# Kernel tuning notes

Measured on AMD Instinct MI355X. Metric: run time of the kernel, lower is better.

Reference implementation:

```python
import jax, jax.numpy as jnp
import numpy as np

B, S, E, H, M, Q = 2, 2048, 768, 12, 768, 4
D = E // H  # head_dim = 64
EPS = 1e-5


def _layernorm(x, g, b):
    m = jnp.mean(x, axis=-1, keepdims=True)
    v = jnp.mean((x - m) ** 2, axis=-1, keepdims=True)
    return (x - m) / jnp.sqrt(v + EPS) * g + b


def setup_inputs() -> dict:
    key = jax.random.key(0)
    ks = jax.random.split(key, 12)
    w = lambda k, shape, s=0.02: (jax.random.normal(k, shape) * s).astype(jnp.float32)
    return {
        "x": jax.random.normal(ks[0], (B, S, E), dtype=jnp.float32),
        "ln1_g": jnp.ones((E,), jnp.float32), "ln1_b": jnp.zeros((E,), jnp.float32),
        "wq": w(ks[1], (E, E)), "bq": jnp.zeros((E,), jnp.float32),
        "wk": w(ks[2], (E, E)), "bk": jnp.zeros((E,), jnp.float32),
        "wv": w(ks[3], (E, E)), "bv": jnp.zeros((E,), jnp.float32),
        "wo": w(ks[4], (E, E)), "bo": jnp.zeros((E,), jnp.float32),
        "ln2_g": jnp.ones((E,), jnp.float32), "ln2_b": jnp.zeros((E,), jnp.float32),
        "w1": w(ks[5], (E, Q * M)), "b1": jnp.zeros((Q * M,), jnp.float32),
        "wvqc": w(ks[6], (M, M)), "bvqc": jnp.zeros((M,), jnp.float32),
        "w2": w(ks[7], (Q * M, E)), "b2": jnp.zeros((E,), jnp.float32),
    }


def reference(x, ln1_g, ln1_b, wq, bq, wk, bk, wv, bv, wo, bo,
              ln2_g, ln2_b, w1, b1, wvqc, bvqc, w2, b2):
    b, s, e = x.shape
    h, d = H, e // H

    # --- attention branch (pre-norm, per-query-L2-normalized logits) ---
    xn = _layernorm(x, ln1_g, ln1_b)
    q = (xn @ wq + bq).reshape(b, s, h, d).transpose(0, 2, 1, 3)  # bhsd
    k = (xn @ wk + bk).reshape(b, s, h, d).transpose(0, 2, 1, 3)
    v = (xn @ wv + bv).reshape(b, s, h, d).transpose(0, 2, 1, 3)

    qk = jnp.einsum('bhsd,bhtd->bhst', q, k)                       # [B,H,S,S]
    q_norm2 = jnp.clip(jnp.sum(q * q, axis=-1, keepdims=True), 1e-5)  # [B,H,S,1]
    logits = qk / jnp.sqrt(d * q_norm2)
    attn = jax.nn.softmax(logits, axis=-1)
    vals = jnp.einsum('bhst,bhtd->bhsd', attn, v)
    vals = vals.transpose(0, 2, 1, 3).reshape(b, s, e)
    x = x + (vals @ wo + bo)  # residual; attn dropout is identity in eval

    # --- quantum-style FeedForward with overlapping q_stride slices ---
    xn2 = _layernorm(x, ln2_g, ln2_b)
    hmid = xn2 @ w1 + b1                                           # [B,S,Q*M]
    m = wvqc.shape[0]
    qstride = w1.shape[1] // m
    # overlapping slices h[..., i:i+M] for i in 0..Q-1, stacked on a new axis
    sl = jnp.stack([hmid[..., i:i + m] for i in range(qstride)], axis=2)  # [B,S,Q,M]
    hv = sl @ wvqc + bvqc                                          # vqc linear
    hv = hv.transpose(0, 1, 3, 2).reshape(b, s, qstride * m)       # interleave
    hv = jax.nn.gelu(hv, approximate=False)
    out = x + (hv @ w2 + b2)
    return out
```

## Files before the change

kernel.cpp:

```cpp
#include <hip/hip_runtime.h>
#include <hip/hip_bf16.h>
#include <math.h>

typedef unsigned short ushort_t;
typedef __attribute__((ext_vector_type(8))) short short8;
typedef __attribute__((ext_vector_type(8))) __bf16 bf16x8;
typedef __attribute__((ext_vector_type(4))) float f32x4;
typedef __attribute__((ext_vector_type(4))) unsigned u32x4;

#define SDIM 2048
#define EDIM 768
#define NTOK 4096

static __device__ __forceinline__ ushort_t f2bf(float f) {
  unsigned u = __builtin_bit_cast(unsigned, f);
  u += 0x7fff + ((u >> 16) & 1);
  return (ushort_t)(u >> 16);
}
static __device__ __forceinline__ float bf2f(ushort_t h) {
  return __builtin_bit_cast(float, (unsigned)h << 16);
}
static __device__ __forceinline__ f32x4 mfma16(short8 a, short8 b, f32x4 c) {
  return __builtin_amdgcn_mfma_f32_16x16x32_bf16(
      __builtin_bit_cast(bf16x8, a), __builtin_bit_cast(bf16x8, b), c, 0, 0, 0);
}
static __device__ __forceinline__ void gload_lds16(const void* g, void* l) {
  __builtin_amdgcn_global_load_lds(
      (const __attribute__((address_space(1))) void*)g,
      (__attribute__((address_space(3))) void*)l, 16, 0, 0);
}
static __device__ __forceinline__ unsigned cvtpk(float lo, float hi) {
  unsigned r;
  asm("v_cvt_pk_bf16_f32 %0, %1, %2" : "=v"(r) : "v"(lo), "v"(hi));
  return r;
}
static __device__ __forceinline__ float exp2fast(float x) {
#if __has_builtin(__builtin_amdgcn_exp2f)
  return __builtin_amdgcn_exp2f(x);
#else
  float r;
  asm("v_exp_f32 %0, %1" : "=v"(r) : "v"(x));
  return r;
#endif
}
static __device__ __forceinline__ float max3f(float a, float b, float c) {
  float r;
  asm("v_max3_f32 %0, %1, %2, %3" : "=v"(r) : "v"(a), "v"(b), "v"(c));
  return r;
}

__global__ void k_castT5(const float* __restrict__ wq, const float* __restrict__ wk,
                         const float* __restrict__ wv, const float* __restrict__ wo,
                         const float* __restrict__ wvqc, ushort_t* __restrict__ oqkv,
                         ushort_t* __restrict__ owo, ushort_t* __restrict__ ovqc) {
  __shared__ float tile[32][33];
  const int z = blockIdx.z;
  const float* in = z == 0 ? wq : z == 1 ? wk : z == 2 ? wv : z == 3 ? wo : wvqc;
  ushort_t* out = z < 3 ? oqkv + (size_t)z * 768 * 768 : (z == 3 ? owo : ovqc);
  int c0 = blockIdx.x * 32, r0 = blockIdx.y * 32;
  int tx = threadIdx.x, ty = threadIdx.y;
#pragma unroll
  for (int i = 0; i < 32; i += 8)
    tile[ty + i][tx] = in[(size_t)(r0 + ty + i) * 768 + c0 + tx];
  __syncthreads();
#pragma unroll
  for (int i = 0; i < 32; i += 8)
    out[(size_t)(c0 + ty + i) * 768 + r0 + tx] = f2bf(tile[tx][ty + i]);
}

__global__ void k_castT(const float* __restrict__ in, ushort_t* __restrict__ out,
                        int R, int C) {
  __shared__ float tile[32][33];
  int c0 = blockIdx.x * 32, r0 = blockIdx.y * 32;
  int tx = threadIdx.x, ty = threadIdx.y;
#pragma unroll
  for (int i = 0; i < 32; i += 8)
    tile[ty + i][tx] = in[(size_t)(r0 + ty + i) * C + c0 + tx];
  __syncthreads();
#pragma unroll
  for (int i = 0; i < 32; i += 8)
    out[(size_t)(c0 + ty + i) * R + r0 + tx] = f2bf(tile[tx][ty + i]);
}

__global__ void k_vT(const ushort_t* __restrict__ in, ushort_t* __restrict__ out) {
  __shared__ ushort_t tile[32][34];
  int bh = blockIdx.z;
  int t0 = blockIdx.x * 32, d0 = blockIdx.y * 32;
  const ushort_t* ib = in + (size_t)bh * SDIM * 64;
  ushort_t* ob = out + (size_t)bh * 64 * SDIM;
  int tx = threadIdx.x, ty = threadIdx.y;
#pragma unroll
  for (int i = 0; i < 32; i += 8)
    tile[ty + i][tx] = ib[(size_t)(t0 + ty + i) * 64 + d0 + tx];
  __syncthreads();
  const int T = t0 + tx, tb = T & ~63, tl = T & 63;
  const int tperm =
      tb + 32 * (tl >> 5) + 8 * ((tl >> 2) & 3) + 4 * ((tl >> 4) & 1) + (tl & 3);
#pragma unroll
  for (int i = 0; i < 32; i += 8)
    ob[(size_t)(d0 + ty + i) * SDIM + tperm] = tile[tx][ty + i];
}

__global__ void k_w1shift(const float* __restrict__ w1, ushort_t* __restrict__ w1s) {
  int idx = blockIdx.x * 256 + threadIdx.x;
  int e = idx / 768, m = idx - (idx / 768) * 768;
#pragma unroll
  for (int i = 0; i < 4; i++)
    w1s[((size_t)i * 768 + e) * 768 + m] = f2bf(w1[(size_t)e * 3072 + i + m]);
}

__global__ __launch_bounds__(256) void k_b1eff(const float* __restrict__ b1,
                                               const ushort_t* __restrict__ wvqcT,
                                               const float* __restrict__ bvqc,
                                               float* __restrict__ b1e) {
  const int n = blockIdx.x;
  const int i = n & 3, j = n >> 2;
  const int t = threadIdx.x;
  float s = 0.f;
  for (int m = t; m < 768; m += 256)
    s += b1[i + m] * bf2f(wvqcT[(size_t)j * 768 + m]);
#pragma unroll
  for (int mm = 32; mm; mm >>= 1) s += __shfl_xor(s, mm);
  __shared__ float red[4];
  if ((t & 63) == 0) red[t >> 6] = s;
  __syncthreads();
  if (t == 0) b1e[n] = red[0] + red[1] + red[2] + red[3] + bvqc[j];
}

__global__ __launch_bounds__(256) void k_ln(const float* __restrict__ x,
                                            const float* __restrict__ gam,
                                            const float* __restrict__ bet,
                                            ushort_t* __restrict__ out) {
  const int row = blockIdx.x, t = threadIdx.x;
  const float* xr = x + (size_t)row * EDIM;
  float v0 = xr[t], v1 = xr[t + 256], v2 = xr[t + 512];
  float s = v0 + v1 + v2;
  float s2 = v0 * v0 + v1 * v1 + v2 * v2;
#pragma unroll
  for (int m = 32; m; m >>= 1) { s += __shfl_xor(s, m); s2 += __shfl_xor(s2, m); }
  __shared__ float red[8];
  const int wid = t >> 6, lane = t & 63;
  if (lane == 0) { red[wid] = s; red[4 + wid] = s2; }
  __syncthreads();
  s = red[0] + red[1] + red[2] + red[3];
  s2 = red[4] + red[5] + red[6] + red[7];
  float mean = s * (1.f / EDIM);
  float var = s2 * (1.f / EDIM) - mean * mean;
  float rstd = rsqrtf(var + 1e-5f);
  ushort_t* orow = out + (size_t)row * EDIM;
  orow[t] = f2bf((v0 - mean) * rstd * gam[t] + bet[t]);
  orow[t + 256] = f2bf((v1 - mean) * rstd * gam[t + 256] + bet[t + 256]);
  orow[t + 512] = f2bf((v2 - mean) * rstd * gam[t + 512] + bet[t + 512]);
}

__global__ __launch_bounds__(256) void k_qscale(const ushort_t* __restrict__ q,
                                                float* __restrict__ qs) {
  const int lane = threadIdx.x & 63, w = threadIdx.x >> 6;
  const int row = blockIdx.x * 4 + w;
  float v = bf2f(q[(size_t)row * 64 + lane]);
  float s = v * v;
#pragma unroll
  for (int m = 32; m; m >>= 1) s += __shfl_xor(s, m);
  if (lane == 0) qs[row] = rsqrtf(64.f * fmaxf(s, 1e-5f));
}

template <int MODE, int BM, int BN>
__global__ __launch_bounds__(256) void k_gemm(
    const ushort_t* __restrict__ A, const ushort_t* __restrict__ Bt, int lda,
    int ldb, int kc, const float* __restrict__ b0, const float* __restrict__ b1p,
    const float* __restrict__ b2p, float* __restrict__ outF,
    const float* __restrict__ resid, ushort_t* __restrict__ o0,
    ushort_t* __restrict__ o1, ushort_t* __restrict__ o2, int ldc) {
  constexpr int MT = BM / 32, NT = BN / 32;
  constexpr int NPA = BM / 32, NPB = BN / 32;
  __shared__ ushort_t As[2][BM * 64];
  __shared__ ushort_t Bs[2][BN * 64];
  const int t = threadIdx.x;
  const int m0 = blockIdx.x * BM, n0 = blockIdx.y * BN;
  if (MODE == 3) Bt += (size_t)blockIdx.z * 768 * 768;
  const int rowa = t >> 3;
  const int gseg = ((t & 7) ^ (rowa & 7)) * 8;
  const ushort_t* ga = A + (size_t)(m0 + rowa) * lda + gseg;
  const ushort_t* gb = Bt + (size_t)(n0 + rowa) * ldb + gseg;
  const int ldst = t * 8;
  const int lane = t & 63, wid = t >> 6;
  const int g = lane >> 4, c = lane & 15;
  const int wm = (wid >> 1) * (BM / 2), wn = (wid & 1) * (BN / 2);
  const int swz = (c & 7) * 8;
  f32x4 acc[MT][NT] = {};

#define STAGE(BUF, K0)                                                           \
  {                                                                              \
    _Pragma("unroll") for (int p = 0; p < NPA; p++)                              \
        gload_lds16(ga + (K0) + (size_t)(p * 32) * lda, As[BUF] + p * 2048 + ldst);\
    _Pragma("unroll") for (int p = 0; p < NPB; p++)                              \
        gload_lds16(gb + (K0) + (size_t)(p * 32) * ldb, Bs[BUF] + p * 2048 + ldst);\
  }

  STAGE(0, 0);
  __syncthreads();
  int cur = 0;
  for (int k0 = 0; k0 < kc; k0 += 64) {
    if (k0 + 64 < kc) STAGE(cur ^ 1, k0 + 64);
    short8 af[2][MT], bfr[2][NT];
#pragma unroll
    for (int kk = 0; kk < 2; kk++) {
#pragma unroll
      for (int mt = 0; mt < MT; mt++)
        af[kk][mt] = *(const short8*)(As[cur] + (wm + mt * 16 + c) * 64 +
                                      ((g * 8 + kk * 32) ^ swz));
#pragma unroll
      for (int nt = 0; nt < NT; nt++)
        bfr[kk][nt] = *(const short8*)(Bs[cur] + (wn + nt * 16 + c) * 64 +
                                       ((g * 8 + kk * 32) ^ swz));
    }
    __builtin_amdgcn_s_setprio(1);
#pragma unroll
    for (int kk = 0; kk < 2; kk++)
#pragma unroll
      for (int mt = 0; mt < MT; mt++)
#pragma unroll
        for (int nt = 0; nt < NT; nt++)
          acc[mt][nt] = mfma16(af[kk][mt], bfr[kk][nt], acc[mt][nt]);
    __builtin_amdgcn_s_setprio(0);
    __syncthreads();
    cur ^= 1;
  }
#undef STAGE

#pragma unroll
  for (int mt = 0; mt < MT; mt++) {
#pragma unroll
    for (int nt = 0; nt < NT; nt++) {
#pragma unroll
      for (int r = 0; r < 4; r++) {
        int row = m0 + wm + mt * 16 + g * 4 + r;
        int col = n0 + wn + nt * 16 + c;
        float val = acc[mt][nt][r];
        if constexpr (MODE == 0) {
          int which = col / 768;
          int nn = col - which * 768;
          int h = nn >> 6, d = nn & 63;
          int bb = row >> 11, s = row & 2047;
          const float* bp = which == 0 ? b0 : (which == 1 ? b1p : b2p);
          ushort_t* dp = which == 0 ? o0 : (which == 1 ? o1 : o2);
          dp[(((size_t)(bb * 12 + h)) * SDIM + s) * 64 + d] = f2bf(val + bp[nn]);
        } else if constexpr (MODE == 1) {
          size_t o = (size_t)row * ldc + col;
          outF[o] = resid[o] + val + b0[col];
        } else if constexpr (MODE == 2) {
          float xg = val + b0[col];
          float z2 = xg * (1.5957691216f + 0.0713548162f * xg * xg);
          float ge = xg / (1.f + __expf(-z2));
          o0[(size_t)row * ldc + col] = f2bf(ge);
        } else {
          o0[((size_t)row * 4 + blockIdx.z) * ldc + col] = f2bf(val);
        }
      }
    }
  }
}

__global__ __launch_bounds__(256) void k_attn(const ushort_t* __restrict__ q,
                                              const ushort_t* __restrict__ k,
                                              const ushort_t* __restrict__ vt,
                                              const float* __restrict__ qs,
                                              ushort_t* __restrict__ vals) {
  const int tid = threadIdx.x;
  const int wid = tid >> 6, lane = tid & 63;
  const int g = lane >> 4, c = lane & 15;
  const int bh = blockIdx.y;
  const int q0 = blockIdx.x * 64 + wid * 16;
  const int bb = bh / 12, h = bh - bb * 12;
  const ushort_t* qb = q + (size_t)bh * SDIM * 64;
  const ushort_t* kb = k + (size_t)bh * SDIM * 64;
  const ushort_t* vb = vt + (size_t)bh * 64 * SDIM;

  __shared__ ushort_t Ks[2][64 * 64];
  __shared__ ushort_t Vs[2][64 * 64];

  const float scq = qs[bh * SDIM + q0 + c] * 1.44269504089f;
  short8 a0 = *(const short8*)(qb + (size_t)(q0 + c) * 64 + g * 8);
  short8 a1 = *(const short8*)(qb + (size_t)(q0 + c) * 64 + 32 + g * 8);
  short8 bq0, bq1;
#pragma unroll
  for (int j = 0; j < 8; j++) {
    bq0[j] = (short)f2bf(bf2f((ushort_t)a0[j]) * scq);
    bq1[j] = (short)f2bf(bf2f((ushort_t)a1[j]) * scq);
  }
  const short8 ones = {0x3F80, 0x3F80, 0x3F80, 0x3F80,
                       0x3F80, 0x3F80, 0x3F80, 0x3F80};

  const int srow = tid >> 3, sj = tid & 7;

#define STAGE(BUF, T0)                                                          \
  {                                                                             \
    _Pragma("unroll") for (int n = 0; n < 2; n++) {                             \
      const int row = n * 32 + srow;                                            \
      const int scol = (sj ^ (row & 7)) * 8;                                    \
      gload_lds16(kb + (size_t)((T0) + row) * 64 + scol,                        \
                  Ks[BUF] + n * 2048 + tid * 8);                                \
      gload_lds16(vb + (size_t)row * SDIM + (T0) + scol,                        \
                  Vs[BUF] + n * 2048 + tid * 8);                                \
    }                                                                           \
  }

  f32x4 accO[4] = {};
  f32x4 accL = {};
  float mr = 0.f;
  float negmr = 0.f;
  const int sw = (c & 7) << 4;

  STAGE(0, 0);
  __syncthreads();
  int cur = 0;
  for (int t0 = 0; t0 < SDIM; t0 += 64) {
    if (t0 + 64 < SDIM) STAGE(cur ^ 1, t0 + 64);
    const char* Kc = (const char*)Ks[cur];
    const char* Vc = (const char*)Vs[cur];
    f32x4 s[4];
#pragma unroll
    for (int i = 0; i < 4; i++) s[i] = {negmr, negmr, negmr, negmr};
    __builtin_amdgcn_s_setprio(1);
#pragma unroll
    for (int i = 0; i < 4; i++) {
      const int rb = (i * 16 + c) * 128;
      short8 ka0 = *(const short8*)(Kc + rb + ((g * 16) ^ sw));
      short8 ka1 = *(const short8*)(Kc + rb + ((64 + g * 16) ^ sw));
      s[i] = mfma16(ka0, bq0, s[i]);
      s[i] = mfma16(ka1, bq1, s[i]);
    }
    __builtin_amdgcn_s_setprio(0);
    float pm = max3f(s[0][0], s[0][1], s[0][2]);
    pm = max3f(pm, s[0][3], s[1][0]);
    pm = max3f(pm, s[1][1], s[1][2]);
    pm = max3f(pm, s[1][3], s[2][0]);
    pm = max3f(pm, s[2][1], s[2][2]);
    pm = max3f(pm, s[2][3], s[3][0]);
    pm = max3f(pm, s[3][1], s[3][2]);
    pm = fmaxf(pm, s[3][3]);
    if (__any(pm > 12.f)) {
      pm = fmaxf(pm, __shfl_xor(pm, 16));
      pm = fmaxf(pm, __shfl_xor(pm, 32));
      float delta = fmaxf(pm, 0.f);
      mr += delta;
      negmr = -mr;
      float al = exp2fast(-delta);
#pragma unroll
      for (int i = 0; i < 4; i++)
#pragma unroll
        for (int r = 0; r < 4; r++) s[i][r] -= delta;
#pragma unroll
      for (int r = 0; r < 4; r++) {
        float alr = __shfl(al, (lane & 0x30) | ((lane >> 4) * 4 + r));
#pragma unroll
        for (int dt = 0; dt < 4; dt++) accO[dt][r] *= alr;
        accL[r] *= alr;
      }
    }
    u32x4 w0 = {cvtpk(exp2fast(s[0][0]), exp2fast(s[0][1])),
                cvtpk(exp2fast(s[0][2]), exp2fast(s[0][3])),
                cvtpk(exp2fast(s[1][0]), exp2fast(s[1][1])),
                cvtpk(exp2fast(s[1][2]), exp2fast(s[1][3]))};
    u32x4 w1 = {cvtpk(exp2fast(s[2][0]), exp2fast(s[2][1])),
                cvtpk(exp2fast(s[2][2]), exp2fast(s[2][3])),
                cvtpk(exp2fast(s[3][0]), exp2fast(s[3][1])),
                cvtpk(exp2fast(s[3][2]), exp2fast(s[3][3]))};
    short8 pa0 = __builtin_bit_cast(short8, w0);
    short8 pa1 = __builtin_bit_cast(short8, w1);
    __builtin_amdgcn_s_setprio(1);
    accL = mfma16(pa0, ones, accL);
    accL = mfma16(pa1, ones, accL);
#pragma unroll
    for (int dt = 0; dt < 4; dt++) {
      const int vbse = (dt * 16 + c) * 128;
      short8 v0 = *(const short8*)(Vc + vbse + ((g * 16) ^ sw));
      short8 v1 = *(const short8*)(Vc + vbse + ((64 + g * 16) ^ sw));
      accO[dt] = mfma16(pa0, v0, accO[dt]);
      accO[dt] = mfma16(pa1, v1, accO[dt]);
    }
    __builtin_amdgcn_s_setprio(0);
    __syncthreads();
    cur ^= 1;
  }
#undef STAGE

  float invr[4];
#pragma unroll
  for (int r = 0; r < 4; r++) invr[r] = 1.f / accL[r];
#pragma unroll
  for (int dt = 0; dt < 4; dt++)
#pragma unroll
    for (int r = 0; r < 4; r++) {
      int s = q0 + 4 * g + r;
      float val = accO[dt][r] * invr[r];
      vals[((size_t)(bb * SDIM + s)) * EDIM + h * 64 + dt * 16 + c] = f2bf(val);
    }
}

extern "C" void kernel_launch(void* const* d_in, const int* in_sizes, int n_in,
                              void* d_out, int out_size, void* d_ws, size_t ws_size,
                              hipStream_t stream) {
  const float* x = (const float*)d_in[0];
  const float* ln1g = (const float*)d_in[1];
  const float* ln1b = (const float*)d_in[2];
  const float* wq = (const float*)d_in[3];
  const float* bq = (const float*)d_in[4];
  const float* wk = (const float*)d_in[5];
  const float* bk = (const float*)d_in[6];
  const float* wv = (const float*)d_in[7];
  const float* bv = (const float*)d_in[8];
  const float* wo = (const float*)d_in[9];
  const float* bo = (const float*)d_in[10];
  const float* ln2g = (const float*)d_in[11];
  const float* ln2b = (const float*)d_in[12];
  const float* w1 = (const float*)d_in[13];
  const float* b1 = (const float*)d_in[14];
  const float* wvqc = (const float*)d_in[15];
  const float* bvqc = (const float*)d_in[16];
  const float* w2 = (const float*)d_in[17];
  const float* b2 = (const float*)d_in[18];
  float* out = (float*)d_out;

  char* w = (char*)d_ws;
  ushort_t* xn = (ushort_t*)(w + 0);
  ushort_t* vtb = (ushort_t*)(w + 0);
  ushort_t* xn2 = (ushort_t*)(w + 6291456);
  float* x2 = (float*)(w + 12582912);
  ushort_t* qb = (ushort_t*)(w + 25165824);
  ushort_t* kb = (ushort_t*)(w + 31457280);
  ushort_t* vb = (ushort_t*)(w + 37748736);
  ushort_t* vals = (ushort_t*)(w + 44040192);
  ushort_t* G = (ushort_t*)(w + 25165824);
  float* qsc = (float*)(w + 50331648);
  ushort_t* wqkvT = (ushort_t*)(w + 50528256);
  ushort_t* woT = (ushort_t*)(w + 54067200);
  ushort_t* wvqcT = (ushort_t*)(w + 55246848);
  ushort_t* w1s = (ushort_t*)(w + 56426496);
  ushort_t* W1eT = (ushort_t*)(w + 61145088);
  float* b1e = (float*)(w + 65863680);
  ushort_t* w2T = (ushort_t*)(w + 65875968);

  dim3 tb(32, 8);
  k_castT5<<<dim3(24, 24, 5), tb, 0, stream>>>(wq, wk, wv, wo, wvqc, wqkvT, woT,
                                               wvqcT);
  k_castT<<<dim3(24, 96), tb, 0, stream>>>(w2, w2T, 3072, 768);
  k_w1shift<<<2304, 256, 0, stream>>>(w1, w1s);
  k_b1eff<<<3072, 256, 0, stream>>>(b1, wvqcT, bvqc, b1e);
  k_gemm<3, 128, 128><<<dim3(6, 6, 4), 256, 0, stream>>>(
      wvqcT, w1s, 768, 768, 768, nullptr, nullptr, nullptr, nullptr, nullptr,
      W1eT, nullptr, nullptr, 768);
  k_ln<<<4096, 256, 0, stream>>>(x, ln1g, ln1b, xn);
  k_gemm<0, 128, 128><<<dim3(32, 18), 256, 0, stream>>>(
      xn, wqkvT, 768, 768, 768, bq, bk, bv, nullptr, nullptr, qb, kb, vb, 0);
  k_vT<<<dim3(64, 2, 24), tb, 0, stream>>>(vb, vtb);
  k_qscale<<<12288, 256, 0, stream>>>(qb, qsc);
  k_attn<<<dim3(32, 24), 256, 0, stream>>>(qb, kb, vtb, qsc, vals);
  k_gemm<1, 64, 64><<<dim3(64, 12), 256, 0, stream>>>(
      vals, woT, 768, 768, 768, bo, nullptr, nullptr, x2, x, nullptr, nullptr,
      nullptr, 768);
  k_ln<<<4096, 256, 0, stream>>>(x2, ln2g, ln2b, xn2);
  k_gemm<2, 128, 128><<<dim3(32, 24), 256, 0, stream>>>(
      xn2, W1eT, 768, 768, 768, b1e, nullptr, nullptr, nullptr, nullptr, G,
      nullptr, nullptr, 3072);
  k_gemm<1, 64, 64><<<dim3(64, 12), 256, 0, stream>>>(
      G, w2T, 3072, 3072, 3072, b2, nullptr, nullptr, out, x2, nullptr, nullptr,
      nullptr, 768);
}
```

Baseline: 217.7 us.

## Split attention over key halves, drop online max, add BK template to GEMM

New measurement: 212.0 us. 1.03x faster.

```diff
diff --git a/kernel.cpp b/kernel.cpp
--- a/kernel.cpp
+++ b/kernel.cpp
@@ -35,17 +35,8 @@
   return r;
 }
 static __device__ __forceinline__ float exp2fast(float x) {
-#if __has_builtin(__builtin_amdgcn_exp2f)
-  return __builtin_amdgcn_exp2f(x);
-#else
   float r;
   asm("v_exp_f32 %0, %1" : "=v"(r) : "v"(x));
-  return r;
-#endif
-}
-static __device__ __forceinline__ float max3f(float a, float b, float c) {
-  float r;
-  asm("v_max3_f32 %0, %1, %2, %3" : "=v"(r) : "v"(a), "v"(b), "v"(c));
   return r;
 }
 
@@ -164,7 +155,7 @@
   if (lane == 0) qs[row] = rsqrtf(64.f * fmaxf(s, 1e-5f));
 }
 
-template <int MODE, int BM, int BN>
+template <int MODE, int BM, int BN, int BK>
 __global__ __launch_bounds__(256) void k_gemm(
     const ushort_t* __restrict__ A, const ushort_t* __restrict__ Bt, int lda,
     int ldb, int kc, const float* __restrict__ b0, const float* __restrict__ b1p,
@@ -172,51 +163,58 @@
     const float* __restrict__ resid, ushort_t* __restrict__ o0,
     ushort_t* __restrict__ o1, ushort_t* __restrict__ o2, int ldc) {
   constexpr int MT = BM / 32, NT = BN / 32;
-  constexpr int NPA = BM / 32, NPB = BN / 32;
-  __shared__ ushort_t As[2][BM * 64];
-  __shared__ ushort_t Bs[2][BN * 64];
+  constexpr int KCH = BK / 8;
+  constexpr int NPA = BM * BK / 2048;
+  constexpr int NPB = BN * BK / 2048;
+  constexpr int ROWSP = 2048 / BK;
+  constexpr int KK = BK / 32;
+  __shared__ ushort_t As[2][BM * BK];
+  __shared__ ushort_t Bs[2][BN * BK];
   const int t = threadIdx.x;
   const int m0 = blockIdx.x * BM, n0 = blockIdx.y * BN;
   if (MODE == 3) Bt += (size_t)blockIdx.z * 768 * 768;
-  const int rowa = t >> 3;
-  const int gseg = ((t & 7) ^ (rowa & 7)) * 8;
-  const ushort_t* ga = A + (size_t)(m0 + rowa) * lda + gseg;
-  const ushort_t* gb = Bt + (size_t)(n0 + rowa) * ldb + gseg;
+  const int srow = t / KCH, sch = t % KCH;
+  const int xs = (BK == 64) ? (srow & 7) : ((srow >> 1) & 3);
+  const int gseg = (sch ^ xs) * 8;
+  const ushort_t* ga = A + (size_t)(m0 + srow) * lda + gseg;
+  const ushort_t* gb = Bt + (size_t)(n0 + srow) * ldb + gseg;
   const int ldst = t * 8;
   const int lane = t & 63, wid = t >> 6;
   const int g = lane >> 4, c = lane & 15;
   const int wm = (wid >> 1) * (BM / 2), wn = (wid & 1) * (BN / 2);
-  const int swz = (c & 7) * 8;
+  const int xc = (BK == 64) ? (c & 7) : ((c >> 1) & 3);
   f32x4 acc[MT][NT] = {};
 
 #define STAGE(BUF, K0)                                                           \
   {                                                                              \
     _Pragma("unroll") for (int p = 0; p < NPA; p++)                              \
-        gload_lds16(ga + (K0) + (size_t)(p * 32) * lda, As[BUF] + p * 2048 + ldst);\
+        gload_lds16(ga + (K0) + (size_t)(p * ROWSP) * lda,                       \
+                    As[BUF] + p * 2048 + ldst);                                  \
     _Pragma("unroll") for (int p = 0; p < NPB; p++)                              \
-        gload_lds16(gb + (K0) + (size_t)(p * 32) * ldb, Bs[BUF] + p * 2048 + ldst);\
+        gload_lds16(gb + (K0) + (size_t)(p * ROWSP) * ldb,                       \
+                    Bs[BUF] + p * 2048 + ldst);                                  \
   }
 
   STAGE(0, 0);
   __syncthreads();
   int cur = 0;
-  for (int k0 = 0; k0 < kc; k0 += 64) {
-    if (k0 + 64 < kc) STAGE(cur ^ 1, k0 + 64);
-    short8 af[2][MT], bfr[2][NT];
-#pragma unroll
-    for (int kk = 0; kk < 2; kk++) {
+  for (int k0 = 0; k0 < kc; k0 += BK) {
+    if (k0 + BK < kc) STAGE(cur ^ 1, k0 + BK);
+    short8 af[KK][MT], bfr[KK][NT];
+#pragma unroll
+    for (int kk = 0; kk < KK; kk++) {
 #pragma unroll
       for (int mt = 0; mt < MT; mt++)
-        af[kk][mt] = *(const short8*)(As[cur] + (wm + mt * 16 + c) * 64 +
-                                      ((g * 8 + kk * 32) ^ swz));
+        af[kk][mt] = *(const short8*)(As[cur] + (wm + mt * 16 + c) * BK +
+                                      (((g + kk * 4) ^ xc) * 8));
 #pragma unroll
       for (int nt = 0; nt < NT; nt++)
-        bfr[kk][nt] = *(const short8*)(Bs[cur] + (wn + nt * 16 + c) * 64 +
-                                       ((g * 8 + kk * 32) ^ swz));
+        bfr[kk][nt] = *(const short8*)(Bs[cur] + (wn + nt * 16 + c) * BK +
+                                       (((g + kk * 4) ^ xc) * 8));
     }
     __builtin_amdgcn_s_setprio(1);
 #pragma unroll
-    for (int kk = 0; kk < 2; kk++)
+    for (int kk = 0; kk < KK; kk++)
 #pragma unroll
       for (int mt = 0; mt < MT; mt++)
 #pragma unroll
@@ -261,15 +259,17 @@
   }
 }
 
-__global__ __launch_bounds__(256) void k_attn(const ushort_t* __restrict__ q,
-                                              const ushort_t* __restrict__ k,
-                                              const ushort_t* __restrict__ vt,
-                                              const float* __restrict__ qs,
-                                              ushort_t* __restrict__ vals) {
+__global__ __launch_bounds__(256) void k_attn(
+    const ushort_t* __restrict__ q, const ushort_t* __restrict__ k,
+    const ushort_t* __restrict__ vt, const float* __restrict__ qs,
+    ushort_t* __restrict__ o0p, ushort_t* __restrict__ o1p,
+    float* __restrict__ lpart) {
   const int tid = threadIdx.x;
   const int wid = tid >> 6, lane = tid & 63;
   const int g = lane >> 4, c = lane & 15;
   const int bh = blockIdx.y;
+  const int z = blockIdx.z;
+  const int tbase = z * (SDIM / 2);
   const int q0 = blockIdx.x * 64 + wid * 16;
   const int bb = bh / 12, h = bh - bb * 12;
   const ushort_t* qb = q + (size_t)bh * SDIM * 64;
@@ -307,20 +307,17 @@
 
   f32x4 accO[4] = {};
   f32x4 accL = {};
-  float mr = 0.f;
-  float negmr = 0.f;
   const int sw = (c & 7) << 4;
 
-  STAGE(0, 0);
+  STAGE(0, tbase);
   __syncthreads();
   int cur = 0;
-  for (int t0 = 0; t0 < SDIM; t0 += 64) {
-    if (t0 + 64 < SDIM) STAGE(cur ^ 1, t0 + 64);
+  for (int tt = 0; tt < SDIM / 128; tt++) {
+    const int t0 = tbase + tt * 64;
+    if (tt + 1 < SDIM / 128) STAGE(cur ^ 1, t0 + 64);
     const char* Kc = (const char*)Ks[cur];
     const char* Vc = (const char*)Vs[cur];
-    f32x4 s[4];
-#pragma unroll
-    for (int i = 0; i < 4; i++) s[i] = {negmr, negmr, negmr, negmr};
+    f32x4 s[4] = {};
     __builtin_amdgcn_s_setprio(1);
 #pragma unroll
     for (int i = 0; i < 4; i++) {
@@ -331,32 +328,12 @@
       s[i] = mfma16(ka1, bq1, s[i]);
     }
     __builtin_amdgcn_s_setprio(0);
-    float pm = max3f(s[0][0], s[0][1], s[0][2]);
-    pm = max3f(pm, s[0][3], s[1][0]);
-    pm = max3f(pm, s[1][1], s[1][2]);
-    pm = max3f(pm, s[1][3], s[2][0]);
-    pm = max3f(pm, s[2][1], s[2][2]);
-    pm = max3f(pm, s[2][3], s[3][0]);
-    pm = max3f(pm, s[3][1], s[3][2]);
-    pm = fmaxf(pm, s[3][3]);
-    if (__any(pm > 12.f)) {
-      pm = fmaxf(pm, __shfl_xor(pm, 16));
-      pm = fmaxf(pm, __shfl_xor(pm, 32));
-      float delta = fmaxf(pm, 0.f);
-      mr += delta;
-      negmr = -mr;
-      float al = exp2fast(-delta);
-#pragma unroll
-      for (int i = 0; i < 4; i++)
-#pragma unroll
-        for (int r = 0; r < 4; r++) s[i][r] -= delta;
-#pragma unroll
-      for (int r = 0; r < 4; r++) {
-        float alr = __shfl(al, (lane & 0x30) | ((lane >> 4) * 4 + r));
-#pragma unroll
-        for (int dt = 0; dt < 4; dt++) accO[dt][r] *= alr;
-        accL[r] *= alr;
-      }
+    short8 v0s[4], v1s[4];
+#pragma unroll
+    for (int dt = 0; dt < 4; dt++) {
+      const int vbse = (dt * 16 + c) * 128;
+      v0s[dt] = *(const short8*)(Vc + vbse + ((g * 16) ^ sw));
+      v1s[dt] = *(const short8*)(Vc + vbse + ((64 + g * 16) ^ sw));
     }
     u32x4 w0 = {cvtpk(exp2fast(s[0][0]), exp2fast(s[0][1])),
                 cvtpk(exp2fast(s[0][2]), exp2fast(s[0][3])),
@@ -373,11 +350,8 @@
     accL = mfma16(pa1, ones, accL);
 #pragma unroll
     for (int dt = 0; dt < 4; dt++) {
-      const int vbse = (dt * 16 + c) * 128;
-      short8 v0 = *(const short8*)(Vc + vbse + ((g * 16) ^ sw));
-      short8 v1 = *(const short8*)(Vc + vbse + ((64 + g * 16) ^ sw));
-      accO[dt] = mfma16(pa0, v0, accO[dt]);
-      accO[dt] = mfma16(pa1, v1, accO[dt]);
+      accO[dt] = mfma16(pa0, v0s[dt], accO[dt]);
+      accO[dt] = mfma16(pa1, v1s[dt], accO[dt]);
     }
     __builtin_amdgcn_s_setprio(0);
     __syncthreads();
@@ -385,17 +359,39 @@
   }
 #undef STAGE
 
-  float invr[4];
-#pragma unroll
-  for (int r = 0; r < 4; r++) invr[r] = 1.f / accL[r];
+  if (c == 0) {
+#pragma unroll
+    for (int r = 0; r < 4; r++)
+      lpart[((size_t)z * 24 + bh) * SDIM + q0 + 4 * g + r] = accL[r];
+  }
+  ushort_t* op = z ? o1p : o0p;
 #pragma unroll
   for (int dt = 0; dt < 4; dt++)
 #pragma unroll
     for (int r = 0; r < 4; r++) {
       int s = q0 + 4 * g + r;
-      float val = accO[dt][r] * invr[r];
-      vals[((size_t)(bb * SDIM + s)) * EDIM + h * 64 + dt * 16 + c] = f2bf(val);
-    }
+      op[((size_t)(bb * SDIM + s)) * EDIM + h * 64 + dt * 16 + c] =
+          f2bf(accO[dt][r]);
+    }
+}
+
+__global__ __launch_bounds__(256) void k_comb(const ushort_t* __restrict__ o0p,
+                                              const ushort_t* __restrict__ o1p,
+                                              const float* __restrict__ lpart,
+                                              ushort_t* __restrict__ vals) {
+  const int gid = blockIdx.x * 256 + threadIdx.x;
+  const int tok = gid / 96, ch = gid - tok * 96;
+  const int h = ch >> 3;
+  const int bb = tok >> 11, s = tok & 2047;
+  const size_t lrow = (size_t)(bb * 12 + h) * SDIM + s;
+  const float inv = 1.f / (lpart[lrow] + lpart[(size_t)24 * SDIM + lrow]);
+  short8 a = *(const short8*)(o0p + (size_t)gid * 8);
+  short8 b = *(const short8*)(o1p + (size_t)gid * 8);
+  short8 o;
+#pragma unroll
+  for (int j = 0; j < 8; j++)
+    o[j] = (short)f2bf((bf2f((ushort_t)a[j]) + bf2f((ushort_t)b[j])) * inv);
+  *(short8*)(vals + (size_t)gid * 8) = o;
 }
 
 extern "C" void kernel_launch(void* const* d_in, const int* in_sizes, int n_in,
@@ -426,6 +422,7 @@
   ushort_t* xn = (ushort_t*)(w + 0);
   ushort_t* vtb = (ushort_t*)(w + 0);
   ushort_t* xn2 = (ushort_t*)(w + 6291456);
+  ushort_t* opart1 = (ushort_t*)(w + 6291456);
   float* x2 = (float*)(w + 12582912);
   ushort_t* qb = (ushort_t*)(w + 25165824);
   ushort_t* kb = (ushort_t*)(w + 31457280);
@@ -437,6 +434,7 @@
   ushort_t* woT = (ushort_t*)(w + 54067200);
   ushort_t* wvqcT = (ushort_t*)(w + 55246848);
   ushort_t* w1s = (ushort_t*)(w + 56426496);
+  float* lpart = (float*)(w + 56426496);
   ushort_t* W1eT = (ushort_t*)(w + 61145088);
   float* b1e = (float*)(w + 65863680);
   ushort_t* w2T = (ushort_t*)(w + 65875968);
@@ -447,23 +445,25 @@
   k_castT<<<dim3(24, 96), tb, 0, stream>>>(w2, w2T, 3072, 768);
   k_w1shift<<<2304, 256, 0, stream>>>(w1, w1s);
   k_b1eff<<<3072, 256, 0, stream>>>(b1, wvqcT, bvqc, b1e);
-  k_gemm<3, 128, 128><<<dim3(6, 6, 4), 256, 0, stream>>>(
+  k_gemm<3, 128, 128, 32><<<dim3(6, 6, 4), 256, 0, stream>>>(
       wvqcT, w1s, 768, 768, 768, nullptr, nullptr, nullptr, nullptr, nullptr,
       W1eT, nullptr, nullptr, 768);
   k_ln<<<4096, 256, 0, stream>>>(x, ln1g, ln1b, xn);
-  k_gemm<0, 128, 128><<<dim3(32, 18), 256, 0, stream>>>(
+  k_gemm<0, 128, 128, 32><<<dim3(32, 18), 256, 0, stream>>>(
       xn, wqkvT, 768, 768, 768, bq, bk, bv, nullptr, nullptr, qb, kb, vb, 0);
   k_vT<<<dim3(64, 2, 24), tb, 0, stream>>>(vb, vtb);
   k_qscale<<<12288, 256, 0, stream>>>(qb, qsc);
-  k_attn<<<dim3(32, 24), 256, 0, stream>>>(qb, kb, vtb, qsc, vals);
-  k_gemm<1, 64, 64><<<dim3(64, 12), 256, 0, stream>>>(
+  k_attn<<<dim3(32, 24, 2), 256, 0, stream>>>(qb, kb, vtb, qsc, vals, opart1,
+                                              lpart);
+  k_comb<<<1536, 256, 0, stream>>>(vals, opart1, lpart, vals);
+  k_gemm<1, 64, 64, 64><<<dim3(64, 12), 256, 0, stream>>>(
       vals, woT, 768, 768, 768, bo, nullptr, nullptr, x2, x, nullptr, nullptr,
       nullptr, 768);
   k_ln<<<4096, 256, 0, stream>>>(x2, ln2g, ln2b, xn2);
-  k_gemm<2, 128, 128><<<dim3(32, 24), 256, 0, stream>>>(
+  k_gemm<2, 128, 128, 32><<<dim3(32, 24), 256, 0, stream>>>(
       xn2, W1eT, 768, 768, 768, b1e, nullptr, nullptr, nullptr, nullptr, G,
       nullptr, nullptr, 3072);
-  k_gemm<1, 64, 64><<<dim3(64, 12), 256, 0, stream>>>(
+  k_gemm<1, 64, 64, 64><<<dim3(64, 12), 256, 0, stream>>>(
       G, w2T, 3072, 3072, 3072, b2, nullptr, nullptr, out, x2, nullptr, nullptr,
       nullptr, 768);
 }
```
